# Optimization experiments

Hardware: AMD Instinct MI355X
Metric: run time of the kernel (lower is better)

## Reference

```python
import jax, jax.numpy as jnp
import numpy as np

N, E, IN, H, L, NB, G = 50000, 300000, 64, 256, 4, 181, 64
EPS = 1e-5
NEG_SLOPE = 0.2


def segment_softmax(e, seg, n):
    m = jax.ops.segment_max(e, seg, num_segments=n)
    a = jnp.exp(e - m[seg])
    d = jax.ops.segment_sum(a, seg, num_segments=n)
    return a / d[seg]


def setup_inputs() -> dict:
    key = jax.random.key(0)
    ks = jax.random.split(key, 32)
    p = lambda k, shape, fan: (jax.random.normal(k, shape, jnp.float32) / np.sqrt(fan)).astype(jnp.float32)
    inp = {}
    inp["x"] = jax.random.normal(ks[0], (N, IN), jnp.float32)
    inp["edge_index"] = jax.random.randint(ks[1], (2, E), 0, N, jnp.int64)
    inp["batch"] = jnp.sort(jax.random.randint(ks[2], (N,), 0, G, jnp.int64))
    inp["W_in"] = p(ks[3], (H, IN), IN); inp["b_in"] = jnp.zeros((H,), jnp.float32)
    inp["Wl"] = p(ks[4], (L, H, H), H); inp["bl"] = jnp.zeros((L, H), jnp.float32)
    inp["Wr"] = p(ks[5], (L, H, H), H); inp["br"] = jnp.zeros((L, H), jnp.float32)
    inp["att"] = p(ks[6], (L, H), H)
    inp["bias_c"] = jnp.zeros((L, H), jnp.float32)
    inp["ln_g"] = jnp.ones((L, H), jnp.float32); inp["ln_b"] = jnp.zeros((L, H), jnp.float32)
    inp["Wg1"] = p(ks[7], (H, H), H); inp["bg1"] = jnp.zeros((H,), jnp.float32)
    inp["Wg2"] = p(ks[8], (1, H), H); inp["bg2"] = jnp.zeros((1,), jnp.float32)
    inp["Ws"] = p(ks[9], (H, H), H); inp["bs"] = jnp.zeros((H,), jnp.float32)
    inp["Wc"] = p(ks[10], (NB, H), H); inp["bc"] = jnp.zeros((NB,), jnp.float32)
    inp["Wr1"] = p(ks[11], (128, H), H); inp["br1"] = jnp.zeros((128,), jnp.float32)
    inp["Wr2"] = p(ks[12], (1, 128), 128); inp["br2"] = jnp.zeros((1,), jnp.float32)
    return inp


def reference(x, edge_index, batch, W_in, b_in, Wl, bl, Wr, br, att, bias_c, ln_g, ln_b,
              Wg1, bg1, Wg2, bg2, Ws, bs, Wc, bc, Wr1, br1, Wr2, br2):
    n = x.shape[0]
    x = x @ W_in.T + b_in  # input projection -> [N,H]
    loops = jnp.arange(n)
    src = jnp.concatenate([edge_index[0], loops])  # GATv2 add_self_loops=True
    dst = jnp.concatenate([edge_index[1], loops])
    for l in range(L):
        x_res = x
        xl = x @ Wl[l].T + bl[l]  # lin_l (source)
        xr = x @ Wr[l].T + br[l]  # lin_r (target)
        h = jax.nn.leaky_relu(xl[src] + xr[dst], NEG_SLOPE)  # [E+N, H]
        e = h @ att[l]                                       # [E+N]
        alpha = segment_softmax(e, dst, n)
        out = jax.ops.segment_sum(alpha[:, None] * xl[src], dst, num_segments=n) + bias_c[l]
        mu = out.mean(-1, keepdims=True)
        var = out.var(-1, keepdims=True)
        out = (out - mu) / jnp.sqrt(var + EPS) * ln_g[l] + ln_b[l]
        x = jax.nn.relu(out) + x_res  # dropout is identity at eval
    gate = jax.nn.relu(x @ Wg1.T + bg1) @ Wg2.T + bg2  # [N,1]
    a = segment_softmax(gate[:, 0], batch, G)
    pooled = jax.ops.segment_sum(a[:, None] * x, batch, num_segments=G)  # [G,H]
    z = jax.nn.relu(pooled @ Ws.T + bs)
    cls_logits = z @ Wc.T + bc                                   # [G,NB]
    residual = jnp.tanh(jax.nn.relu(z @ Wr1.T + br1) @ Wr2.T + br2)[:, 0]  # [G]
    return cls_logits, residual
```

## Files before the change

### kernel.cpp

```cpp
#include <hip/hip_runtime.h>
#include <math.h>

#define N_NODES 50000
#define N_EDGES 300000
#define IN_DIM 64
#define H 256
#define LAYERS 4
#define NB 181
#define NGRAPH 64
#define EE (N_EDGES + N_NODES)
#define NEG_SLOPE 0.2f
#define LN_EPS 1e-5f

typedef unsigned short u16;
typedef __attribute__((ext_vector_type(8))) _Float16 half8;
typedef __attribute__((ext_vector_type(2))) _Float16 half2v;
typedef __attribute__((ext_vector_type(4))) float floatx4;

__device__ __forceinline__ u16 f2h(float f) {
  _Float16 h = (_Float16)f;
  return __builtin_bit_cast(u16, h);
}
__device__ __forceinline__ float h2f(u16 b) {
  return (float)__builtin_bit_cast(_Float16, b);
}

__device__ __forceinline__ float wave_reduce_sum(float v) {
  #pragma unroll
  for (int off = 32; off > 0; off >>= 1) v += __shfl_xor(v, off, 64);
  return v;
}

__global__ void cast_f16_kernel(const float* __restrict__ in, u16* __restrict__ out, int n4) {
  int i = blockIdx.x * 256 + threadIdx.x;
  if (i < n4) {
    float4 f = ((const float4*)in)[i];
    ushort4 o;
    o.x = f2h(f.x); o.y = f2h(f.y); o.z = f2h(f.z); o.w = f2h(f.w);
    ((ushort4*)out)[i] = o;
  }
}

__global__ void cast_weights_kernel(
    const float* __restrict__ W_in, const float* __restrict__ Wg1,
    const float* __restrict__ Wl, const float* __restrict__ Wr,
    u16* __restrict__ win_h, u16* __restrict__ wg1_h,
    u16* __restrict__ wl_h, u16* __restrict__ wr_h)
{
  int i = blockIdx.x * 256 + threadIdx.x;
  int which = blockIdx.y;
  const float* s; u16* dd; int n4;
  if (which == 0)      { s = W_in; dd = win_h; n4 = H * IN_DIM / 4; }
  else if (which == 1) { s = Wg1;  dd = wg1_h; n4 = H * H / 4; }
  else if (which == 2) { s = Wl;   dd = wl_h;  n4 = LAYERS * H * H / 4; }
  else                 { s = Wr;   dd = wr_h;  n4 = LAYERS * H * H / 4; }
  if (i < n4) {
    float4 f = ((const float4*)s)[i];
    ushort4 o;
    o.x = f2h(f.x); o.y = f2h(f.y); o.z = f2h(f.z); o.w = f2h(f.w);
    ((ushort4*)dd)[i] = o;
  }
}

__global__ void init_counts_kernel(int* __restrict__ cnt) {
  int i = blockIdx.x * 256 + threadIdx.x;
  if (i < N_NODES) cnt[i] = 1;
}

__global__ void count_edges_kernel(const int* __restrict__ dst, int* __restrict__ cnt) {
  int e = blockIdx.x * 256 + threadIdx.x;
  if (e < N_EDGES) atomicAdd(&cnt[dst[e]], 1);
}

__global__ void scan_blocks_kernel(const int* __restrict__ cnt, int* __restrict__ partial,
                                   int* __restrict__ bsums, int n) {
  __shared__ int buf[256];
  int tid = threadIdx.x;
  int i = blockIdx.x * 256 + tid;
  buf[tid] = (i < n) ? cnt[i] : 0;
  __syncthreads();
  #pragma unroll
  for (int off = 1; off < 256; off <<= 1) {
    int t = (tid >= off) ? buf[tid - off] : 0;
    __syncthreads();
    buf[tid] += t;
    __syncthreads();
  }
  if (i < n) partial[i] = buf[tid];
  if (tid == 255) bsums[blockIdx.x] = buf[255];
}

__global__ void scan_sums_kernel(int* __restrict__ bsums, int nblk) {
  __shared__ int buf[256];
  int tid = threadIdx.x;
  buf[tid] = (tid < nblk) ? bsums[tid] : 0;
  __syncthreads();
  #pragma unroll
  for (int off = 1; off < 256; off <<= 1) {
    int t = (tid >= off) ? buf[tid - off] : 0;
    __syncthreads();
    buf[tid] += t;
    __syncthreads();
  }
  if (tid < nblk) bsums[tid] = buf[tid];
}

__global__ void scan_write_kernel(const int* __restrict__ partial, const int* __restrict__ bsums,
                                  int* __restrict__ rowp, int n) {
  int i = blockIdx.x * 256 + threadIdx.x;
  if (i < n) {
    int b = blockIdx.x;
    int off = (b > 0) ? bsums[b - 1] : 0;
    rowp[i + 1] = partial[i] + off;
    if (i == 0) rowp[0] = 0;
  }
}

__global__ void fill_self_kernel(const int* __restrict__ rowp, int* __restrict__ col,
                                 int* __restrict__ fillpos) {
  int i = blockIdx.x * 256 + threadIdx.x;
  if (i < N_NODES) {
    int p = rowp[i];
    col[p] = i;
    fillpos[i] = p + 1;
  }
}

__global__ void fill_edges_kernel(const int* __restrict__ src, const int* __restrict__ dst,
                                  int* __restrict__ fillpos, int* __restrict__ col) {
  int e = blockIdx.x * 256 + threadIdx.x;
  if (e < N_EDGES) {
    int d = dst[e];
    int p = atomicAdd(&fillpos[d], 1);
    col[p] = src[e];
  }
}

#define GTM 128
#define GTK 64
#define LDB 72
#define SSTR 132

__global__ __launch_bounds__(256) void gemm_proj_kernel(
    const u16* __restrict__ A, const u16* __restrict__ W,
    const float* __restrict__ bias, u16* __restrict__ outh, int M, int K)
{
  __shared__ u16 smem[2 * GTM * LDB];
  u16* As = smem;
  u16* Bs = smem + GTM * LDB;
  int tid = threadIdx.x;
  int lane = tid & 63;
  int wave = tid >> 6;
  int wm = (wave >> 1) * 64;
  int wn = (wave & 1) * 64;
  int bm = blockIdx.y * GTM;
  int n0 = blockIdx.x * 128;
  int lr = tid >> 3;
  int lc = (tid & 7) * 8;

  floatx4 zero4 = {0.f, 0.f, 0.f, 0.f};
  floatx4 acc[4][4];
  #pragma unroll
  for (int i = 0; i < 4; i++)
    #pragma unroll
    for (int j = 0; j < 4; j++) acc[i][j] = zero4;

  int q8 = (lane >> 4) * 8;
  int mrow = lane & 15;

  for (int k0 = 0; k0 < K; k0 += GTK) {
    __syncthreads();
    #pragma unroll
    for (int p = 0; p < 4; p++) {
      int row = lr + p * 32;
      int gr = bm + row;
      uint4 av = {0, 0, 0, 0};
      if (gr < M) av = *(const uint4*)&A[(size_t)gr * K + k0 + lc];
      *(uint4*)&As[row * LDB + lc] = av;
      uint4 bv = *(const uint4*)&W[(size_t)(n0 + row) * K + k0 + lc];
      *(uint4*)&Bs[row * LDB + lc] = bv;
    }
    __syncthreads();
    #pragma unroll
    for (int h = 0; h < 2; h++) {
      half8 af[4], bf[4];
      #pragma unroll
      for (int i = 0; i < 4; i++)
        af[i] = *(const half8*)&As[(wm + i * 16 + mrow) * LDB + h * 32 + q8];
      #pragma unroll
      for (int j = 0; j < 4; j++)
        bf[j] = *(const half8*)&Bs[(wn + j * 16 + mrow) * LDB + h * 32 + q8];
      #pragma unroll
      for (int i = 0; i < 4; i++)
        #pragma unroll
        for (int j = 0; j < 4; j++)
          acc[i][j] = __builtin_amdgcn_mfma_f32_16x16x32_f16(af[i], bf[j], acc[i][j], 0, 0, 0);
    }
  }

  __syncthreads();
  u16* stage = smem;
  int ccol = lane & 15;
  int crow4 = (lane >> 4) * 4;
  #pragma unroll
  for (int j = 0; j < 4; j++) {
    float bv = bias[n0 + wn + j * 16 + ccol];
    #pragma unroll
    for (int i = 0; i < 4; i++) {
      #pragma unroll
      for (int r = 0; r < 4; r++) {
        int row = wm + i * 16 + crow4 + r;
        stage[row * SSTR + wn + j * 16 + ccol] = f2h(acc[i][j][r] + bv);
      }
    }
  }
  __syncthreads();
  int rr = tid >> 1;
  int c0 = (tid & 1) * 64;
  int grow = bm + rr;
  if (grow < M) {
    const ushort4* sp = (const ushort4*)&stage[rr * SSTR + c0];
    ushort4* gp = (ushort4*)&outh[(size_t)grow * H + n0 + c0];
    #pragma unroll
    for (int q = 0; q < 16; q++) gp[q] = sp[q];
  }
}

#define DTM 64
#define AST 264
#define SSTR2 132

__global__ __launch_bounds__(256) void gemm_dual2_kernel(
    const u16* __restrict__ A, const u16* __restrict__ Wlb, const u16* __restrict__ Wrb,
    const float* __restrict__ biasL, const float* __restrict__ biasR,
    u16* __restrict__ outL, u16* __restrict__ outR, int M)
{
  __shared__ u16 As[DTM * AST];
  __shared__ u16 Bs[128 * LDB];
  int tid = threadIdx.x;
  int lane = tid & 63;
  int wave = tid >> 6;
  int wn = wave * 32;
  int bm = blockIdx.x * DTM;
  int mrow = lane & 15;
  int q8 = (lane >> 4) * 8;
  int ccol = lane & 15;
  int crow4 = (lane >> 4) * 4;

  {
    int col = (tid & 31) * 8;
    int r0 = tid >> 5;
    #pragma unroll
    for (int it = 0; it < 8; it++) {
      int row = r0 + it * 8;
      int gr = bm + row;
      uint4 av = {0, 0, 0, 0};
      if (gr < M) av = *(const uint4*)&A[(size_t)gr * H + col];
      *(uint4*)&As[row * AST + col] = av;
    }
  }

  floatx4 zero4 = {0.f, 0.f, 0.f, 0.f};

  for (int nt = 0; nt < 4; nt++) {
    const u16* W = (nt < 2) ? Wlb : Wrb;
    const float* bias = (nt < 2) ? biasL : biasR;
    u16* outp = (nt < 2) ? outL : outR;
    int n0 = (nt & 1) * 128;

    floatx4 acc[4][2];
    #pragma unroll
    for (int i = 0; i < 4; i++) {
      acc[i][0] = zero4;
      acc[i][1] = zero4;
    }

    for (int k0 = 0; k0 < H; k0 += 64) {
      __syncthreads();
      {
        int col = (tid & 7) * 8;
        int r0 = tid >> 3;
        #pragma unroll
        for (int p2 = 0; p2 < 4; p2++) {
          int row = r0 + p2 * 32;
          uint4 bv = *(const uint4*)&W[(size_t)(n0 + row) * H + k0 + col];
          *(uint4*)&Bs[row * LDB + col] = bv;
        }
      }
      __syncthreads();
      #pragma unroll
      for (int h = 0; h < 2; h++) {
        half8 af[4], bf[2];
        #pragma unroll
        for (int i = 0; i < 4; i++)
          af[i] = *(const half8*)&As[(i * 16 + mrow) * AST + k0 + h * 32 + q8];
        #pragma unroll
        for (int j = 0; j < 2; j++)
          bf[j] = *(const half8*)&Bs[(wn + j * 16 + mrow) * LDB + h * 32 + q8];
        #pragma unroll
        for (int i = 0; i < 4; i++)
          #pragma unroll
          for (int j = 0; j < 2; j++)
            acc[i][j] = __builtin_amdgcn_mfma_f32_16x16x32_f16(af[i], bf[j], acc[i][j], 0, 0, 0);
      }
    }

    __syncthreads();
    u16* stage = Bs;
    #pragma unroll
    for (int j = 0; j < 2; j++) {
      float bv = bias[n0 + wn + j * 16 + ccol];
      #pragma unroll
      for (int i = 0; i < 4; i++) {
        #pragma unroll
        for (int r = 0; r < 4; r++) {
          int row = i * 16 + crow4 + r;
          stage[row * SSTR2 + wn + j * 16 + ccol] = f2h(acc[i][j][r] + bv);
        }
      }
    }
    __syncthreads();
    {
      int row = tid >> 2;
      int c0 = (tid & 3) * 32;
      int grow = bm + row;
      if (grow < M) {
        #pragma unroll
        for (int q = 0; q < 8; q++)
          *(ushort4*)&outp[(size_t)grow * H + n0 + c0 + q * 4] =
              *(const ushort4*)&stage[row * SSTR2 + c0 + q * 4];
      }
    }
  }
}

__global__ __launch_bounds__(256) void gemm_gate_kernel(
    const u16* __restrict__ A, const u16* __restrict__ W,
    const float* __restrict__ bias, const float* __restrict__ Wg2,
    float* __restrict__ gate, int M)
{
  __shared__ u16 smem[2 * GTM * LDB];
  u16* As = smem;
  u16* Bs = smem + GTM * LDB;
  int tid = threadIdx.x;
  int lane = tid & 63;
  int wave = tid >> 6;
  int wm = (wave >> 1) * 64;
  int wn = (wave & 1) * 64;
  int bm = blockIdx.y * GTM;
  int bn = blockIdx.x * 128;
  int lr = tid >> 3;
  int lc = (tid & 7) * 8;

  floatx4 zero4 = {0.f, 0.f, 0.f, 0.f};
  floatx4 acc[4][4];
  #pragma unroll
  for (int i = 0; i < 4; i++)
    #pragma unroll
    for (int j = 0; j < 4; j++) acc[i][j] = zero4;

  int q8 = (lane >> 4) * 8;
  int mrow = lane & 15;

  for (int k0 = 0; k0 < H; k0 += GTK) {
    __syncthreads();
    #pragma unroll
    for (int p = 0; p < 4; p++) {
      int row = lr + p * 32;
      int gr = bm + row;
      uint4 av = {0, 0, 0, 0};
      if (gr < M) av = *(const uint4*)&A[(size_t)gr * H + k0 + lc];
      *(uint4*)&As[row * LDB + lc] = av;
      uint4 bv = *(const uint4*)&W[(size_t)(bn + row) * H + k0 + lc];
      *(uint4*)&Bs[row * LDB + lc] = bv;
    }
    __syncthreads();
    #pragma unroll
    for (int h = 0; h < 2; h++) {
      half8 af[4], bf[4];
      #pragma unroll
      for (int i = 0; i < 4; i++)
        af[i] = *(const half8*)&As[(wm + i * 16 + mrow) * LDB + h * 32 + q8];
      #pragma unroll
      for (int j = 0; j < 4; j++)
        bf[j] = *(const half8*)&Bs[(wn + j * 16 + mrow) * LDB + h * 32 + q8];
      #pragma unroll
      for (int i = 0; i < 4; i++)
        #pragma unroll
        for (int j = 0; j < 4; j++)
          acc[i][j] = __builtin_amdgcn_mfma_f32_16x16x32_f16(af[i], bf[j], acc[i][j], 0, 0, 0);
    }
  }

  int ccol = lane & 15;
  float bv[4], wv[4];
  #pragma unroll
  for (int j = 0; j < 4; j++) {
    int col = bn + wn + j * 16 + ccol;
    bv[j] = bias[col];
    wv[j] = Wg2[col];
  }
  #pragma unroll
  for (int i = 0; i < 4; i++) {
    #pragma unroll
    for (int r = 0; r < 4; r++) {
      float p = 0.f;
      #pragma unroll
      for (int j = 0; j < 4; j++) {
        float hcol = fmaxf(acc[i][j][r] + bv[j], 0.f);
        p += hcol * wv[j];
      }
      p += __shfl_xor(p, 1, 64);
      p += __shfl_xor(p, 2, 64);
      p += __shfl_xor(p, 4, 64);
      p += __shfl_xor(p, 8, 64);
      int row = bm + wm + i * 16 + (lane >> 4) * 4 + r;
      if ((lane & 15) == 0 && row < M) atomicAdd(&gate[row], p);
    }
  }
}

__global__ __launch_bounds__(256) void layer_fused_kernel(
    const u16* __restrict__ xl, const u16* __restrict__ xr,
    u16* __restrict__ xst,
    const int* __restrict__ rowp, const int* __restrict__ col,
    const float* __restrict__ att, const float* __restrict__ bias_c,
    const float* __restrict__ ln_g, const float* __restrict__ ln_b)
{
  int lane = threadIdx.x & 63;
  int v = blockIdx.x * 4 + (threadIdx.x >> 6);
  if (v >= N_NODES) return;
  int f4 = lane << 2;
  size_t rowbase = (size_t)v * H;
  ushort4 xr4 = *(const ushort4*)&xr[rowbase + f4];
  float xrx = h2f(xr4.x), xry = h2f(xr4.y), xrz = h2f(xr4.z), xrw = h2f(xr4.w);
  float4 attv = *(const float4*)&att[f4];
  int beg = rowp[v], end = rowp[v + 1];
  float m = -INFINITY, d = 0.f;
  float ox = 0.f, oy = 0.f, oz = 0.f, ow = 0.f;
  int p = beg;
  for (; p + 2 <= end; p += 2) {
    int u0 = col[p];
    int u1 = col[p + 1];
    ushort4 a04 = *(const ushort4*)&xl[(size_t)u0 * H + f4];
    ushort4 a14 = *(const ushort4*)&xl[(size_t)u1 * H + f4];
    float a0x = h2f(a04.x), a0y = h2f(a04.y), a0z = h2f(a04.z), a0w = h2f(a04.w);
    float a1x = h2f(a14.x), a1y = h2f(a14.y), a1z = h2f(a14.z), a1w = h2f(a14.w);
    float t0x = a0x + xrx; t0x = t0x > 0.f ? t0x : NEG_SLOPE * t0x;
    float t0y = a0y + xry; t0y = t0y > 0.f ? t0y : NEG_SLOPE * t0y;
    float t0z = a0z + xrz; t0z = t0z > 0.f ? t0z : NEG_SLOPE * t0z;
    float t0w = a0w + xrw; t0w = t0w > 0.f ? t0w : NEG_SLOPE * t0w;
    float t1x = a1x + xrx; t1x = t1x > 0.f ? t1x : NEG_SLOPE * t1x;
    float t1y = a1y + xry; t1y = t1y > 0.f ? t1y : NEG_SLOPE * t1y;
    float t1z = a1z + xrz; t1z = t1z > 0.f ? t1z : NEG_SLOPE * t1z;
    float t1w = a1w + xrw; t1w = t1w > 0.f ? t1w : NEG_SLOPE * t1w;
    float pe0 = t0x * attv.x + t0y * attv.y + t0z * attv.z + t0w * attv.w;
    float pe1 = t1x * attv.x + t1y * attv.y + t1z * attv.z + t1w * attv.w;
    #pragma unroll
    for (int off = 32; off > 0; off >>= 1) {
      pe0 += __shfl_xor(pe0, off, 64);
      pe1 += __shfl_xor(pe1, off, 64);
    }
    float mn = fmaxf(m, fmaxf(pe0, pe1));
    float sc = __expf(m - mn);
    float w0 = __expf(pe0 - mn);
    float w1 = __expf(pe1 - mn);
    d = fmaf(d, sc, w0 + w1);
    ox = fmaf(ox, sc, fmaf(w0, a0x, w1 * a1x));
    oy = fmaf(oy, sc, fmaf(w0, a0y, w1 * a1y));
    oz = fmaf(oz, sc, fmaf(w0, a0z, w1 * a1z));
    ow = fmaf(ow, sc, fmaf(w0, a0w, w1 * a1w));
    m = mn;
  }
  if (p < end) {
    int u0 = col[p];
    ushort4 a04 = *(const ushort4*)&xl[(size_t)u0 * H + f4];
    float a0x = h2f(a04.x), a0y = h2f(a04.y), a0z = h2f(a04.z), a0w = h2f(a04.w);
    float t0x = a0x + xrx; t0x = t0x > 0.f ? t0x : NEG_SLOPE * t0x;
    float t0y = a0y + xry; t0y = t0y > 0.f ? t0y : NEG_SLOPE * t0y;
    float t0z = a0z + xrz; t0z = t0z > 0.f ? t0z : NEG_SLOPE * t0z;
    float t0w = a0w + xrw; t0w = t0w > 0.f ? t0w : NEG_SLOPE * t0w;
    float pe0 = t0x * attv.x + t0y * attv.y + t0z * attv.z + t0w * attv.w;
    pe0 = wave_reduce_sum(pe0);
    float mn = fmaxf(m, pe0);
    float sc = __expf(m - mn);
    float w0 = __expf(pe0 - mn);
    d = fmaf(d, sc, w0);
    ox = fmaf(ox, sc, w0 * a0x);
    oy = fmaf(oy, sc, w0 * a0y);
    oz = fmaf(oz, sc, w0 * a0z);
    ow = fmaf(ow, sc, w0 * a0w);
    m = mn;
  }
  float invd = 1.0f / d;
  float4 bc4 = *(const float4*)&bias_c[f4];
  ox = ox * invd + bc4.x;
  oy = oy * invd + bc4.y;
  oz = oz * invd + bc4.z;
  ow = ow * invd + bc4.w;
  float s = wave_reduce_sum(ox + oy + oz + ow);
  float mean = s * (1.0f / H);
  float cx = ox - mean, cy = oy - mean, cz = oz - mean, cw = ow - mean;
  float sq = wave_reduce_sum(cx * cx + cy * cy + cz * cz + cw * cw);
  float rstd = rsqrtf(sq * (1.0f / H) + LN_EPS);
  float4 g4 = *(const float4*)&ln_g[f4];
  float4 b4 = *(const float4*)&ln_b[f4];
  ushort4 xres4 = *(const ushort4*)&xst[rowbase + f4];
  float yx = fmaxf(fmaf(cx * rstd, g4.x, b4.x), 0.f) + h2f(xres4.x);
  float yy = fmaxf(fmaf(cy * rstd, g4.y, b4.y), 0.f) + h2f(xres4.y);
  float yz = fmaxf(fmaf(cz * rstd, g4.z, b4.z), 0.f) + h2f(xres4.z);
  float yw = fmaxf(fmaf(cw * rstd, g4.w, b4.w), 0.f) + h2f(xres4.w);
  ushort4 yb;
  yb.x = f2h(yx); yb.y = f2h(yy); yb.z = f2h(yz); yb.w = f2h(yw);
  *(ushort4*)&xst[rowbase + f4] = yb;
}

__global__ void gate_init_kernel(float* __restrict__ gate, const float* __restrict__ bg2,
                                 const int* __restrict__ batch,
                                 int* __restrict__ gstart, int* __restrict__ gend) {
  int i = blockIdx.x * 256 + threadIdx.x;
  if (i < N_NODES) {
    gate[i] = bg2[0];
    int b = batch[i];
    if (i == 0 || batch[i - 1] != b) gstart[b] = i;
    if (i == N_NODES - 1 || batch[i + 1] != b) gend[b] = i + 1;
  }
}

__global__ __launch_bounds__(256) void pool_prep_kernel(
    const float* __restrict__ gate, const int* __restrict__ gstart,
    const int* __restrict__ gend, float* __restrict__ gmax, float* __restrict__ gdinv,
    float* __restrict__ pooled)
{
  __shared__ float red[256];
  int g = blockIdx.x, tid = threadIdx.x;
  pooled[(size_t)g * H + tid] = 0.f;
  int s = gstart[g], e = gend[g];
  float lm = -INFINITY;
  for (int i = s + tid; i < e; i += 256) lm = fmaxf(lm, gate[i]);
  red[tid] = lm;
  __syncthreads();
  for (int off = 128; off; off >>= 1) {
    if (tid < off) red[tid] = fmaxf(red[tid], red[tid + off]);
    __syncthreads();
  }
  float m = red[0];
  __syncthreads();
  float lsum = 0.0f;
  for (int i = s + tid; i < e; i += 256) lsum += __expf(gate[i] - m);
  red[tid] = lsum;
  __syncthreads();
  for (int off = 128; off; off >>= 1) {
    if (tid < off) red[tid] += red[tid + off];
    __syncthreads();
  }
  if (tid == 0) {
    gmax[g] = m;
    gdinv[g] = (s < e) ? 1.0f / red[0] : 0.0f;
  }
}

__global__ __launch_bounds__(256) void pool_accum_kernel(
    const float* __restrict__ gate, const u16* __restrict__ xh,
    const int* __restrict__ batch, const float* __restrict__ gmax,
    const float* __restrict__ gdinv, float* __restrict__ pooled)
{
  __shared__ float wl[128];
  __shared__ int gl[128];
  int b0 = blockIdx.x * 128;
  int tid = threadIdx.x;
  if (tid < 128) {
    int v = b0 + tid;
    if (v < N_NODES) {
      int g = batch[v];
      gl[tid] = g;
      wl[tid] = __expf(gate[v] - gmax[g]) * gdinv[g];
    } else {
      gl[tid] = -1;
      wl[tid] = 0.f;
    }
  }
  __syncthreads();
  int cnt = min(128, N_NODES - b0);
  float acc = 0.f;
  int cur = gl[0];
  for (int j = 0; j < cnt; j++) {
    int g = gl[j];
    if (g != cur) {
      atomicAdd(&pooled[(size_t)cur * H + tid], acc);
      acc = 0.f;
      cur = g;
    }
    acc += wl[j] * h2f(xh[(size_t)(b0 + j) * H + tid]);
  }
  if (cur >= 0) atomicAdd(&pooled[(size_t)cur * H + tid], acc);
}

__global__ __launch_bounds__(256) void head_kernel(
    const float* __restrict__ pooled,
    const float* __restrict__ Ws, const float* __restrict__ bs,
    const float* __restrict__ Wc, const float* __restrict__ bc,
    const float* __restrict__ Wr1, const float* __restrict__ br1,
    const float* __restrict__ Wr2, const float* __restrict__ br2,
    float* __restrict__ out)
{
  __shared__ float psh[256];
  __shared__ float zsh[256];
  __shared__ float r1sh[128];
  int g = blockIdx.x, tid = threadIdx.x;
  psh[tid] = pooled[(size_t)g * H + tid];
  __syncthreads();
  {
    float acc = bs[tid];
    const float4* wr = (const float4*)&Ws[(size_t)tid * H];
    for (int k4 = 0; k4 < H / 4; k4++) {
      float4 wv = wr[k4];
      float4 av = *(const float4*)&psh[k4 * 4];
      acc += av.x * wv.x + av.y * wv.y + av.z * wv.z + av.w * wv.w;
    }
    zsh[tid] = fmaxf(acc, 0.f);
  }
  __syncthreads();
  if (tid < NB) {
    float acc = bc[tid];
    const float4* wr = (const float4*)&Wc[(size_t)tid * H];
    for (int k4 = 0; k4 < H / 4; k4++) {
      float4 wv = wr[k4];
      float4 av = *(const float4*)&zsh[k4 * 4];
      acc += av.x * wv.x + av.y * wv.y + av.z * wv.z + av.w * wv.w;
    }
    out[(size_t)g * NB + tid] = acc;
  }
  if (tid < 128) {
    float acc = br1[tid];
    const float4* wr = (const float4*)&Wr1[(size_t)tid * H];
    for (int k4 = 0; k4 < H / 4; k4++) {
      float4 wv = wr[k4];
      float4 av = *(const float4*)&zsh[k4 * 4];
      acc += av.x * wv.x + av.y * wv.y + av.z * wv.z + av.w * wv.w;
    }
    r1sh[tid] = fmaxf(acc, 0.f);
  }
  __syncthreads();
  if (tid < 64) {
    float s2 = r1sh[tid] * Wr2[tid] + r1sh[tid + 64] * Wr2[tid + 64];
    s2 = wave_reduce_sum(s2);
    if (tid == 0) out[(size_t)NGRAPH * NB + g] = tanhf(s2 + br2[0]);
  }
}

extern "C" void kernel_launch(void* const* d_in, const int* in_sizes, int n_in,
                              void* d_out, int out_size, void* d_ws, size_t ws_size,
                              hipStream_t stream) {
  const float* x_in   = (const float*)d_in[0];
  const int*   eidx   = (const int*)d_in[1];
  const int*   batch  = (const int*)d_in[2];
  const float* W_in   = (const float*)d_in[3];
  const float* b_in   = (const float*)d_in[4];
  const float* Wl     = (const float*)d_in[5];
  const float* bl     = (const float*)d_in[6];
  const float* Wr     = (const float*)d_in[7];
  const float* br     = (const float*)d_in[8];
  const float* att    = (const float*)d_in[9];
  const float* bias_c = (const float*)d_in[10];
  const float* ln_g   = (const float*)d_in[11];
  const float* ln_b   = (const float*)d_in[12];
  const float* Wg1    = (const float*)d_in[13];
  const float* bg1    = (const float*)d_in[14];
  const float* Wg2    = (const float*)d_in[15];
  const float* bg2    = (const float*)d_in[16];
  const float* Ws     = (const float*)d_in[17];
  const float* bs     = (const float*)d_in[18];
  const float* Wc     = (const float*)d_in[19];
  const float* bc     = (const float*)d_in[20];
  const float* Wr1    = (const float*)d_in[21];
  const float* br1    = (const float*)d_in[22];
  const float* Wr2    = (const float*)d_in[23];
  const float* br2    = (const float*)d_in[24];
  float* out = (float*)d_out;

  char* w = (char*)d_ws;
  u16* x_h    = (u16*)w;    w += sizeof(u16) * (size_t)N_NODES * H;
  u16* xl_h   = (u16*)w;    w += sizeof(u16) * (size_t)N_NODES * H;
  u16* xr_h   = (u16*)w;    w += sizeof(u16) * (size_t)N_NODES * H;
  u16* xin_h  = (u16*)w;    w += sizeof(u16) * (size_t)N_NODES * IN_DIM;
  u16* win_h  = (u16*)w;    w += sizeof(u16) * (size_t)H * IN_DIM;
  u16* wl_h   = (u16*)w;    w += sizeof(u16) * (size_t)LAYERS * H * H;
  u16* wr_h   = (u16*)w;    w += sizeof(u16) * (size_t)LAYERS * H * H;
  u16* wg1_h  = (u16*)w;    w += sizeof(u16) * (size_t)H * H;
  float* pooled = (float*)w; w += sizeof(float) * NGRAPH * H;
  float* gate = (float*)w;  w += sizeof(float) * N_NODES;
  float* gmax = (float*)w;  w += sizeof(float) * NGRAPH;
  float* gdinv= (float*)w;  w += sizeof(float) * NGRAPH;
  int* cnt    = (int*)w;    w += sizeof(int) * N_NODES;
  int* rowp   = (int*)w;    w += sizeof(int) * (N_NODES + 1);
  int* col    = (int*)w;    w += sizeof(int) * EE;
  int* partial= (int*)w;    w += sizeof(int) * N_NODES;
  int* bsums  = (int*)w;    w += sizeof(int) * 256;
  int* gstart = (int*)w;    w += sizeof(int) * NGRAPH;
  int* gend   = (int*)w;    w += sizeof(int) * NGRAPH;
  (void)ws_size; (void)n_in; (void)in_sizes; (void)out_size;

  const int* src = eidx;
  const int* dst = eidx + N_EDGES;
  int nblkN = (N_NODES + 255) / 256;
  int nblkE = (N_EDGES + 255) / 256;
  int mtiles = (N_NODES + GTM - 1) / GTM;
  int mtiles2 = (N_NODES + DTM - 1) / DTM;

  init_counts_kernel<<<nblkN, 256, 0, stream>>>(cnt);
  count_edges_kernel<<<nblkE, 256, 0, stream>>>(dst, cnt);
  scan_blocks_kernel<<<nblkN, 256, 0, stream>>>(cnt, partial, bsums, N_NODES);
  scan_sums_kernel<<<1, 256, 0, stream>>>(bsums, nblkN);
  scan_write_kernel<<<nblkN, 256, 0, stream>>>(partial, bsums, rowp, N_NODES);
  fill_self_kernel<<<nblkN, 256, 0, stream>>>(rowp, col, cnt);
  fill_edges_kernel<<<nblkE, 256, 0, stream>>>(src, dst, cnt, col);

  {
    int maxn4 = LAYERS * H * H / 4;
    dim3 gcast((maxn4 + 255) / 256, 4);
    cast_weights_kernel<<<gcast, 256, 0, stream>>>(W_in, Wg1, Wl, Wr,
                                                   win_h, wg1_h, wl_h, wr_h);
    int n4 = N_NODES * IN_DIM / 4;
    cast_f16_kernel<<<(n4 + 255) / 256, 256, 0, stream>>>(x_in, xin_h, n4);
  }

  dim3 gproj(2, mtiles);
  gemm_proj_kernel<<<gproj, 256, 0, stream>>>(xin_h, win_h, b_in, x_h, N_NODES, IN_DIM);

  int nblkV = N_NODES / 4;
  for (int l = 0; l < LAYERS; l++) {
    gemm_dual2_kernel<<<mtiles2, 256, 0, stream>>>(x_h,
        wl_h + (size_t)l * H * H, wr_h + (size_t)l * H * H,
        bl + l * H, br + l * H, xl_h, xr_h, N_NODES);
    layer_fused_kernel<<<nblkV, 256, 0, stream>>>(xl_h, xr_h, x_h, rowp, col,
        att + l * H, bias_c + l * H, ln_g + l * H, ln_b + l * H);
  }

  gate_init_kernel<<<nblkN, 256, 0, stream>>>(gate, bg2, batch, gstart, gend);
  dim3 ggate(2, mtiles);
  gemm_gate_kernel<<<ggate, 256, 0, stream>>>(x_h, wg1_h, bg1, Wg2, gate, N_NODES);

  pool_prep_kernel<<<NGRAPH, 256, 0, stream>>>(gate, gstart, gend, gmax, gdinv, pooled);
  pool_accum_kernel<<<(N_NODES + 127) / 128, 256, 0, stream>>>(gate, x_h, batch, gmax, gdinv, pooled);

  head_kernel<<<NGRAPH, 256, 0, stream>>>(pooled, Ws, bs, Wc, bc, Wr1, br1, Wr2, br2, out);
}
```

Before: 631.3 us.

## Register-prefetch GEMM weight tiles and unroll edge aggregation by four

The dual GEMM kernel now loads the next weight K-tile, or the first tile of the next output block, into registers while the current tile is being used, so global loads overlap the MFMA work. The fused GATv2 aggregation loop handles four neighbours per iteration with masked tails instead of two plus a scalar remainder, which exposes more independent gathers and shuffle reductions. The price is higher register pressure, plus wasted loads and exp calls on padded lanes for nodes with few edges.

```diff
diff --git a/kernel.cpp b/kernel.cpp
--- a/kernel.cpp
+++ b/kernel.cpp
@@ -14,7 +14,6 @@
 
 typedef unsigned short u16;
 typedef __attribute__((ext_vector_type(8))) _Float16 half8;
-typedef __attribute__((ext_vector_type(2))) _Float16 half2v;
 typedef __attribute__((ext_vector_type(4))) float floatx4;
 
 __device__ __forceinline__ u16 f2h(float f) {
@@ -246,6 +245,8 @@
   int q8 = (lane >> 4) * 8;
   int ccol = lane & 15;
   int crow4 = (lane >> 4) * 4;
+  int colB = (tid & 7) * 8;
+  int r0B = tid >> 3;
 
   {
     int col = (tid & 31) * 8;
@@ -262,10 +263,15 @@
 
   floatx4 zero4 = {0.f, 0.f, 0.f, 0.f};
 
+  uint4 rB[4];
+  #pragma unroll
+  for (int p2 = 0; p2 < 4; p2++)
+    rB[p2] = *(const uint4*)&Wlb[(size_t)(r0B + p2 * 32) * H + colB];
+
   for (int nt = 0; nt < 4; nt++) {
-    const u16* W = (nt < 2) ? Wlb : Wrb;
     const float* bias = (nt < 2) ? biasL : biasR;
     u16* outp = (nt < 2) ? outL : outR;
+    const u16* W = (nt < 2) ? Wlb : Wrb;
     int n0 = (nt & 1) * 128;
 
     floatx4 acc[4][2];
@@ -275,17 +281,21 @@
       acc[i][1] = zero4;
     }
 
-    for (int k0 = 0; k0 < H; k0 += 64) {
+    for (int kk = 0; kk < 4; kk++) {
       __syncthreads();
-      {
-        int col = (tid & 7) * 8;
-        int r0 = tid >> 3;
-        #pragma unroll
-        for (int p2 = 0; p2 < 4; p2++) {
-          int row = r0 + p2 * 32;
-          uint4 bv = *(const uint4*)&W[(size_t)(n0 + row) * H + k0 + col];
-          *(uint4*)&Bs[row * LDB + col] = bv;
-        }
+      #pragma unroll
+      for (int p2 = 0; p2 < 4; p2++)
+        *(uint4*)&Bs[(r0B + p2 * 32) * LDB + colB] = rB[p2];
+      if (kk < 3) {
+        #pragma unroll
+        for (int p2 = 0; p2 < 4; p2++)
+          rB[p2] = *(const uint4*)&W[(size_t)(n0 + r0B + p2 * 32) * H + (kk + 1) * 64 + colB];
+      } else if (nt < 3) {
+        const u16* Wn = (nt + 1 < 2) ? Wlb : Wrb;
+        int n0n = ((nt + 1) & 1) * 128;
+        #pragma unroll
+        for (int p2 = 0; p2 < 4; p2++)
+          rB[p2] = *(const uint4*)&Wn[(size_t)(n0n + r0B + p2 * 32) * H + colB];
       }
       __syncthreads();
       #pragma unroll
@@ -293,7 +303,7 @@
         half8 af[4], bf[2];
         #pragma unroll
         for (int i = 0; i < 4; i++)
-          af[i] = *(const half8*)&As[(i * 16 + mrow) * AST + k0 + h * 32 + q8];
+          af[i] = *(const half8*)&As[(i * 16 + mrow) * AST + kk * 64 + h * 32 + q8];
         #pragma unroll
         for (int j = 0; j < 2; j++)
           bf[j] = *(const half8*)&Bs[(wn + j * 16 + mrow) * LDB + h * 32 + q8];
@@ -438,60 +448,63 @@
   int beg = rowp[v], end = rowp[v + 1];
   float m = -INFINITY, d = 0.f;
   float ox = 0.f, oy = 0.f, oz = 0.f, ow = 0.f;
-  int p = beg;
-  for (; p + 2 <= end; p += 2) {
+
+  for (int p = beg; p < end; p += 4) {
+    int n = end - p;
     int u0 = col[p];
-    int u1 = col[p + 1];
-    ushort4 a04 = *(const ushort4*)&xl[(size_t)u0 * H + f4];
-    ushort4 a14 = *(const ushort4*)&xl[(size_t)u1 * H + f4];
-    float a0x = h2f(a04.x), a0y = h2f(a04.y), a0z = h2f(a04.z), a0w = h2f(a04.w);
-    float a1x = h2f(a14.x), a1y = h2f(a14.y), a1z = h2f(a14.z), a1w = h2f(a14.w);
-    float t0x = a0x + xrx; t0x = t0x > 0.f ? t0x : NEG_SLOPE * t0x;
-    float t0y = a0y + xry; t0y = t0y > 0.f ? t0y : NEG_SLOPE * t0y;
-    float t0z = a0z + xrz; t0z = t0z > 0.f ? t0z : NEG_SLOPE * t0z;
-    float t0w = a0w + xrw; t0w = t0w > 0.f ? t0w : NEG_SLOPE * t0w;
-    float t1x = a1x + xrx; t1x = t1x > 0.f ? t1x : NEG_SLOPE * t1x;
-    float t1y = a1y + xry; t1y = t1y > 0.f ? t1y : NEG_SLOPE * t1y;
-    float t1z = a1z + xrz; t1z = t1z > 0.f ? t1z : NEG_SLOPE * t1z;
-    float t1w = a1w + xrw; t1w = t1w > 0.f ? t1w : NEG_SLOPE * t1w;
-    float pe0 = t0x * attv.x + t0y * attv.y + t0z * attv.z + t0w * attv.w;
-    float pe1 = t1x * attv.x + t1y * attv.y + t1z * attv.z + t1w * attv.w;
+    int u1 = (n > 1) ? col[p + 1] : u0;
+    int u2 = (n > 2) ? col[p + 2] : u0;
+    int u3 = (n > 3) ? col[p + 3] : u0;
+    ushort4 A0 = *(const ushort4*)&xl[(size_t)u0 * H + f4];
+    ushort4 A1 = *(const ushort4*)&xl[(size_t)u1 * H + f4];
+    ushort4 A2 = *(const ushort4*)&xl[(size_t)u2 * H + f4];
+    ushort4 A3 = *(const ushort4*)&xl[(size_t)u3 * H + f4];
+    float a0x = h2f(A0.x), a0y = h2f(A0.y), a0z = h2f(A0.z), a0w = h2f(A0.w);
+    float a1x = h2f(A1.x), a1y = h2f(A1.y), a1z = h2f(A1.z), a1w = h2f(A1.w);
+    float a2x = h2f(A2.x), a2y = h2f(A2.y), a2z = h2f(A2.z), a2w = h2f(A2.w);
+    float a3x = h2f(A3.x), a3y = h2f(A3.y), a3z = h2f(A3.z), a3w = h2f(A3.w);
+    float t;
+    float pe0, pe1, pe2, pe3;
+    t = a0x + xrx; t = t > 0.f ? t : NEG_SLOPE * t; pe0 = t * attv.x;
+    t = a0y + xry; t = t > 0.f ? t : NEG_SLOPE * t; pe0 = fmaf(t, attv.y, pe0);
+    t = a0z + xrz; t = t > 0.f ? t : NEG_SLOPE * t; pe0 = fmaf(t, attv.z, pe0);
+    t = a0w + xrw; t = t > 0.f ? t : NEG_SLOPE * t; pe0 = fmaf(t, attv.w, pe0);
+    t = a1x + xrx; t = t > 0.f ? t : NEG_SLOPE * t; pe1 = t * attv.x;
+    t = a1y + xry; t = t > 0.f ? t : NEG_SLOPE * t; pe1 = fmaf(t, attv.y, pe1);
+    t = a1z + xrz; t = t > 0.f ? t : NEG_SLOPE * t; pe1 = fmaf(t, attv.z, pe1);
+    t = a1w + xrw; t = t > 0.f ? t : NEG_SLOPE * t; pe1 = fmaf(t, attv.w, pe1);
+    t = a2x + xrx; t = t > 0.f ? t : NEG_SLOPE * t; pe2 = t * attv.x;
+    t = a2y + xry; t = t > 0.f ? t : NEG_SLOPE * t; pe2 = fmaf(t, attv.y, pe2);
+    t = a2z + xrz; t = t > 0.f ? t : NEG_SLOPE * t; pe2 = fmaf(t, attv.z, pe2);
+    t = a2w + xrw; t = t > 0.f ? t : NEG_SLOPE * t; pe2 = fmaf(t, attv.w, pe2);
+    t = a3x + xrx; t = t > 0.f ? t : NEG_SLOPE * t; pe3 = t * attv.x;
+    t = a3y + xry; t = t > 0.f ? t : NEG_SLOPE * t; pe3 = fmaf(t, attv.y, pe3);
+    t = a3z + xrz; t = t > 0.f ? t : NEG_SLOPE * t; pe3 = fmaf(t, attv.z, pe3);
+    t = a3w + xrw; t = t > 0.f ? t : NEG_SLOPE * t; pe3 = fmaf(t, attv.w, pe3);
     #pragma unroll
     for (int off = 32; off > 0; off >>= 1) {
       pe0 += __shfl_xor(pe0, off, 64);
       pe1 += __shfl_xor(pe1, off, 64);
-    }
-    float mn = fmaxf(m, fmaxf(pe0, pe1));
+      pe2 += __shfl_xor(pe2, off, 64);
+      pe3 += __shfl_xor(pe3, off, 64);
+    }
+    pe1 = (n > 1) ? pe1 : -INFINITY;
+    pe2 = (n > 2) ? pe2 : -INFINITY;
+    pe3 = (n > 3) ? pe3 : -INFINITY;
+    float mn = fmaxf(fmaxf(fmaxf(pe0, pe1), fmaxf(pe2, pe3)), m);
     float sc = __expf(m - mn);
     float w0 = __expf(pe0 - mn);
     float w1 = __expf(pe1 - mn);
-    d = fmaf(d, sc, w0 + w1);
-    ox = fmaf(ox, sc, fmaf(w0, a0x, w1 * a1x));
-    oy = fmaf(oy, sc, fmaf(w0, a0y, w1 * a1y));
-    oz = fmaf(oz, sc, fmaf(w0, a0z, w1 * a1z));
-    ow = fmaf(ow, sc, fmaf(w0, a0w, w1 * a1w));
+    float w2 = __expf(pe2 - mn);
+    float w3 = __expf(pe3 - mn);
+    d = fmaf(d, sc, (w0 + w1) + (w2 + w3));
+    ox = fmaf(ox, sc, fmaf(w0, a0x, fmaf(w1, a1x, fmaf(w2, a2x, w3 * a3x))));
+    oy = fmaf(oy, sc, fmaf(w0, a0y, fmaf(w1, a1y, fmaf(w2, a2y, w3 * a3y))));
+    oz = fmaf(oz, sc, fmaf(w0, a0z, fmaf(w1, a1z, fmaf(w2, a2z, w3 * a3z))));
+    ow = fmaf(ow, sc, fmaf(w0, a0w, fmaf(w1, a1w, fmaf(w2, a2w, w3 * a3w))));
     m = mn;
   }
-  if (p < end) {
-    int u0 = col[p];
-    ushort4 a04 = *(const ushort4*)&xl[(size_t)u0 * H + f4];
-    float a0x = h2f(a04.x), a0y = h2f(a04.y), a0z = h2f(a04.z), a0w = h2f(a04.w);
-    float t0x = a0x + xrx; t0x = t0x > 0.f ? t0x : NEG_SLOPE * t0x;
-    float t0y = a0y + xry; t0y = t0y > 0.f ? t0y : NEG_SLOPE * t0y;
-    float t0z = a0z + xrz; t0z = t0z > 0.f ? t0z : NEG_SLOPE * t0z;
-    float t0w = a0w + xrw; t0w = t0w > 0.f ? t0w : NEG_SLOPE * t0w;
-    float pe0 = t0x * attv.x + t0y * attv.y + t0z * attv.z + t0w * attv.w;
-    pe0 = wave_reduce_sum(pe0);
-    float mn = fmaxf(m, pe0);
-    float sc = __expf(m - mn);
-    float w0 = __expf(pe0 - mn);
-    d = fmaf(d, sc, w0);
-    ox = fmaf(ox, sc, w0 * a0x);
-    oy = fmaf(oy, sc, w0 * a0y);
-    oz = fmaf(oz, sc, w0 * a0z);
-    ow = fmaf(ow, sc, w0 * a0w);
-    m = mn;
-  }
+
   float invd = 1.0f / d;
   float4 bc4 = *(const float4*)&bias_c[f4];
   ox = ox * invd + bc4.x;
```

Measured after the change: 821.5 us. 30.1% more time.

## Split dual GEMM N-tiles across grid blocks and stream A tiles per K step

Applied to the files above, without the earlier changes.

The dual Wl/Wr projection GEMM previously had each block load a full 64x256 A tile once and loop over four 128-column output tiles. Now each of the four N-tiles gets its own block in a 2D grid, and A is loaded in 64-column K chunks alongside B. This gives four times more blocks for occupancy and latency hiding and uses a smaller shared-memory footprint per block. The cost is re-reading A from global memory or L2 four times. Output stores are also widened to 16-byte writes.

```diff
diff --git a/kernel.cpp b/kernel.cpp
--- a/kernel.cpp
+++ b/kernel.cpp
@@ -14,7 +14,6 @@
 
 typedef unsigned short u16;
 typedef __attribute__((ext_vector_type(8))) _Float16 half8;
-typedef __attribute__((ext_vector_type(2))) _Float16 half2v;
 typedef __attribute__((ext_vector_type(4))) float floatx4;
 
 __device__ __forceinline__ u16 f2h(float f) {
@@ -227,109 +226,97 @@
 }
 
 #define DTM 64
-#define AST 264
 #define SSTR2 132
 
-__global__ __launch_bounds__(256) void gemm_dual2_kernel(
+__global__ __launch_bounds__(256) void gemm_dual3_kernel(
     const u16* __restrict__ A, const u16* __restrict__ Wlb, const u16* __restrict__ Wrb,
     const float* __restrict__ biasL, const float* __restrict__ biasR,
     u16* __restrict__ outL, u16* __restrict__ outR, int M)
 {
-  __shared__ u16 As[DTM * AST];
+  __shared__ u16 As[DTM * LDB];
   __shared__ u16 Bs[128 * LDB];
   int tid = threadIdx.x;
   int lane = tid & 63;
   int wave = tid >> 6;
   int wn = wave * 32;
-  int bm = blockIdx.x * DTM;
+  int nt = blockIdx.x;
+  int bm = blockIdx.y * DTM;
+  const u16* W = (nt < 2) ? Wlb : Wrb;
+  const float* bias = (nt < 2) ? biasL : biasR;
+  u16* outp = (nt < 2) ? outL : outR;
+  int n0 = (nt & 1) * 128;
   int mrow = lane & 15;
   int q8 = (lane >> 4) * 8;
   int ccol = lane & 15;
   int crow4 = (lane >> 4) * 4;
-
-  {
-    int col = (tid & 31) * 8;
-    int r0 = tid >> 5;
-    #pragma unroll
-    for (int it = 0; it < 8; it++) {
-      int row = r0 + it * 8;
+  int lr = tid >> 3;
+  int lc = (tid & 7) * 8;
+
+  floatx4 zero4 = {0.f, 0.f, 0.f, 0.f};
+  floatx4 acc[4][2];
+  #pragma unroll
+  for (int i = 0; i < 4; i++) {
+    acc[i][0] = zero4;
+    acc[i][1] = zero4;
+  }
+
+  for (int k0 = 0; k0 < H; k0 += 64) {
+    __syncthreads();
+    #pragma unroll
+    for (int p = 0; p < 2; p++) {
+      int row = lr + p * 32;
       int gr = bm + row;
       uint4 av = {0, 0, 0, 0};
-      if (gr < M) av = *(const uint4*)&A[(size_t)gr * H + col];
-      *(uint4*)&As[row * AST + col] = av;
-    }
-  }
-
-  floatx4 zero4 = {0.f, 0.f, 0.f, 0.f};
-
-  for (int nt = 0; nt < 4; nt++) {
-    const u16* W = (nt < 2) ? Wlb : Wrb;
-    const float* bias = (nt < 2) ? biasL : biasR;
-    u16* outp = (nt < 2) ? outL : outR;
-    int n0 = (nt & 1) * 128;
-
-    floatx4 acc[4][2];
-    #pragma unroll
-    for (int i = 0; i < 4; i++) {
-      acc[i][0] = zero4;
-      acc[i][1] = zero4;
-    }
-
-    for (int k0 = 0; k0 < H; k0 += 64) {
-      __syncthreads();
-      {
-        int col = (tid & 7) * 8;
-        int r0 = tid >> 3;
-        #pragma unroll
-        for (int p2 = 0; p2 < 4; p2++) {
-          int row = r0 + p2 * 32;
-          uint4 bv = *(const uint4*)&W[(size_t)(n0 + row) * H + k0 + col];
-          *(uint4*)&Bs[row * LDB + col] = bv;
-        }
-      }
-      __syncthreads();
-      #pragma unroll
-      for (int h = 0; h < 2; h++) {
-        half8 af[4], bf[2];
-        #pragma unroll
-        for (int i = 0; i < 4; i++)
-          af[i] = *(const half8*)&As[(i * 16 + mrow) * AST + k0 + h * 32 + q8];
+      if (gr < M) av = *(const uint4*)&A[(size_t)gr * H + k0 + lc];
+      *(uint4*)&As[row * LDB + lc] = av;
+    }
+    #pragma unroll
+    for (int p = 0; p < 4; p++) {
+      int row = lr + p * 32;
+      uint4 bv = *(const uint4*)&W[(size_t)(n0 + row) * H + k0 + lc];
+      *(uint4*)&Bs[row * LDB + lc] = bv;
+    }
+    __syncthreads();
+    #pragma unroll
+    for (int h = 0; h < 2; h++) {
+      half8 af[4], bf[2];
+      #pragma unroll
+      for (int i = 0; i < 4; i++)
+        af[i] = *(const half8*)&As[(i * 16 + mrow) * LDB + h * 32 + q8];
+      #pragma unroll
+      for (int j = 0; j < 2; j++)
+        bf[j] = *(const half8*)&Bs[(wn + j * 16 + mrow) * LDB + h * 32 + q8];
+      #pragma unroll
+      for (int i = 0; i < 4; i++)
         #pragma unroll
         for (int j = 0; j < 2; j++)
-          bf[j] = *(const half8*)&Bs[(wn + j * 16 + mrow) * LDB + h * 32 + q8];
-        #pragma unroll
-        for (int i = 0; i < 4; i++)
-          #pragma unroll
-          for (int j = 0; j < 2; j++)
-            acc[i][j] = __builtin_amdgcn_mfma_f32_16x16x32_f16(af[i], bf[j], acc[i][j], 0, 0, 0);
+          acc[i][j] = __builtin_amdgcn_mfma_f32_16x16x32_f16(af[i], bf[j], acc[i][j], 0, 0, 0);
+    }
+  }
+
+  __syncthreads();
+  u16* stage = Bs;
+  #pragma unroll
+  for (int j = 0; j < 2; j++) {
+    float bv = bias[n0 + wn + j * 16 + ccol];
+    #pragma unroll
+    for (int i = 0; i < 4; i++) {
+      #pragma unroll
+      for (int r = 0; r < 4; r++) {
+        int row = i * 16 + crow4 + r;
+        stage[row * SSTR2 + wn + j * 16 + ccol] = f2h(acc[i][j][r] + bv);
       }
     }
-
-    __syncthreads();
-    u16* stage = Bs;
-    #pragma unroll
-    for (int j = 0; j < 2; j++) {
-      float bv = bias[n0 + wn + j * 16 + ccol];
-      #pragma unroll
-      for (int i = 0; i < 4; i++) {
-        #pragma unroll
-        for (int r = 0; r < 4; r++) {
-          int row = i * 16 + crow4 + r;
-          stage[row * SSTR2 + wn + j * 16 + ccol] = f2h(acc[i][j][r] + bv);
-        }
-      }
-    }
-    __syncthreads();
-    {
-      int row = tid >> 2;
-      int c0 = (tid & 3) * 32;
-      int grow = bm + row;
-      if (grow < M) {
-        #pragma unroll
-        for (int q = 0; q < 8; q++)
-          *(ushort4*)&outp[(size_t)grow * H + n0 + c0 + q * 4] =
-              *(const ushort4*)&stage[row * SSTR2 + c0 + q * 4];
-      }
+  }
+  __syncthreads();
+  #pragma unroll
+  for (int pass = 0; pass < 4; pass++) {
+    int row = pass * 16 + (tid >> 4);
+    int cu = (tid & 15) * 8;
+    int grow = bm + row;
+    if (grow < M) {
+      *(uint4*)&outp[(size_t)grow * H + n0 + cu] =
+          *(const uint4*)&stage[row * SSTR2 + cu];
     }
   }
 }
@@ -729,8 +716,9 @@
   gemm_proj_kernel<<<gproj, 256, 0, stream>>>(xin_h, win_h, b_in, x_h, N_NODES, IN_DIM);
 
   int nblkV = N_NODES / 4;
+  dim3 gdual(4, mtiles2);
   for (int l = 0; l < LAYERS; l++) {
-    gemm_dual2_kernel<<<mtiles2, 256, 0, stream>>>(x_h,
+    gemm_dual3_kernel<<<gdual, 256, 0, stream>>>(x_h,
         wl_h + (size_t)l * H * H, wr_h + (size_t)l * H * H,
         bl + l * H, br + l * H, xl_h, xr_h, N_NODES);
     layer_fused_kernel<<<nblkV, 256, 0, stream>>>(xl_h, xr_h, x_h, rowp, col,
```

After: 600.3 us. 1.05x faster.
